# Kernel tuning notes

Hardware: AMD Instinct MI355X
Metric: run time of the kernel (lower is better)

## Reference

```python
import jax, jax.numpy as jnp
import numpy as np

N, C, P, M = 8, 20, 8732, 16
THRESHOLD, NEG_POS_RATIO, ALPHA = 0.5, 3, 1.0


def cxcy_to_xy(c):
    return jnp.concatenate([c[..., :2] - c[..., 2:] / 2.0, c[..., :2] + c[..., 2:] / 2.0], axis=-1)


def xy_to_cxcy(xy):
    return jnp.concatenate([(xy[..., :2] + xy[..., 2:]) / 2.0, xy[..., 2:] - xy[..., :2]], axis=-1)


def cxcy_to_gcxgcy(cxcy, priors):
    g_cxcy = (cxcy[..., :2] - priors[..., :2]) / (priors[..., 2:] / 10.0)
    g_wh = jnp.log(cxcy[..., 2:] / priors[..., 2:]) * 5.0
    return jnp.concatenate([g_cxcy, g_wh], axis=-1)


def jaccard(a, b):
    # a: (M,4), b: (P,4), boundary coords -> IoU (M,P)
    lo = jnp.maximum(a[:, None, :2], b[None, :, :2])
    hi = jnp.minimum(a[:, None, 2:], b[None, :, 2:])
    inter = jnp.prod(jnp.clip(hi - lo, 0.0), axis=-1)
    area_a = jnp.prod(a[:, 2:] - a[:, :2], axis=-1)
    area_b = jnp.prod(b[:, 2:] - b[:, :2], axis=-1)
    return inter / (area_a[:, None] + area_b[None, :] - inter)


def setup_inputs() -> dict:
    key = jax.random.key(0)
    k1, k2, k3, k4, k5, k6 = jax.random.split(key, 6)
    predicted_locs = jax.random.normal(k1, (N, C, P, 4), jnp.float32)
    predicted_scores = jax.random.normal(k2, (N, C, P, 2), jnp.float32)
    # valid ground-truth boundary boxes (x1<x2, y1<y2) in [0,1]
    ctr = jax.random.uniform(k3, (N, C, M, 2), minval=0.2, maxval=0.8)
    wh = jax.random.uniform(k4, (N, C, M, 2), minval=0.05, maxval=0.3)
    boxes = jnp.concatenate([ctr - wh / 2.0, ctr + wh / 2.0], axis=-1)
    # valid priors in cxcywh (w,h > 0 so log-encoding is finite)
    pctr = jax.random.uniform(k5, (P, 2), minval=0.05, maxval=0.95)
    pwh = jax.random.uniform(k6, (P, 2), minval=0.05, maxval=0.5)
    priors_cxcy = jnp.concatenate([pctr, pwh], axis=-1)
    labels = jnp.ones((N, C, M), jnp.int32)  # binary per-class head: object label = 1
    return {
        "predicted_locs": predicted_locs,
        "predicted_scores": predicted_scores,
        "boxes": boxes,
        "labels": labels,
        "priors_cxcy": priors_cxcy,
    }


def _forward(predicted_locs, predicted_scores, boxes, priors_cxcy, labels):
    n_classes = predicted_scores.shape[1]
    n_priors = predicted_scores.shape[2]
    priors_xy = cxcy_to_xy(priors_cxcy)

    def match(b, lab):
        # b: (M,4) boundary, lab: (M,) int
        ov = jaccard(b, priors_xy)                       # (M,P)
        obj_for_prior = jnp.argmax(ov, axis=0)           # (P,)
        ov_for_prior = jnp.max(ov, axis=0)               # (P,)
        prior_for_obj = jnp.argmax(ov, axis=1)           # (M,)
        # force each object to own its best prior
        obj_for_prior = obj_for_prior.at[prior_for_obj].set(jnp.arange(b.shape[0]))
        ov_for_prior = ov_for_prior.at[prior_for_obj].set(1.0)
        cls = jnp.where(ov_for_prior < THRESHOLD, 0, lab[obj_for_prior])  # (P,)
        tl = cxcy_to_gcxgcy(xy_to_cxcy(b[obj_for_prior]), priors_cxcy)    # (P,4)
        return tl, cls

    true_locs, true_classes = jax.vmap(jax.vmap(match))(boxes, labels)  # (N,C,P,4), (N,C,P)

    pos = true_classes != 0                      # (N,C,P)
    posf = pos.astype(predicted_locs.dtype)
    n_pos_bc = posf.sum(axis=2)                  # (N,C) positives per image per class
    n_pos_c = n_pos_bc.sum(axis=0)               # (C,)

    # localization: mean L1 over positive priors (4 coords each), per class
    l1 = jnp.abs(predicted_locs - true_locs).sum(-1) * posf   # (N,C,P)
    loc_loss_c = l1.sum(axis=(0, 2)) / jnp.maximum(n_pos_c * 4.0, 1.0)

    # per-prior binary cross entropy
    logp = jax.nn.log_softmax(predicted_scores, axis=-1)      # (N,C,P,2)
    ce = -jnp.take_along_axis(logp, true_classes[..., None], axis=-1)[..., 0]  # (N,C,P)
    conf_pos_c = (ce * posf).sum(axis=(0, 2))

    # hard negative mining: sort negatives desc per (image,class) row, keep top 3*n_pos
    ce_neg = jnp.where(pos, 0.0, ce)
    ce_neg_sorted = -jnp.sort(-ce_neg, axis=-1)               # (N,C,P) descending
    n_hard = NEG_POS_RATIO * n_pos_bc                         # (N,C)
    ranks = jnp.arange(n_priors, dtype=n_hard.dtype)
    hard_mask = ranks[None, None, :] < n_hard[..., None]
    conf_hard_c = (ce_neg_sorted * hard_mask).sum(axis=(0, 2))

    safe = jnp.maximum(n_pos_c, 1.0)
    loss_c = jnp.where(
        n_pos_c > 0,
        (conf_pos_c + conf_hard_c + ALPHA * loc_loss_c) / safe,
        0.0,
    ) / n_classes
    return loss_c.sum()


def reference(predicted_locs, predicted_scores, boxes, labels, priors_cxcy):
    return _forward(predicted_locs, predicted_scores, boxes, priors_cxcy, labels)
```

## Files before the change

### kernel.cpp

```cpp
#include <hip/hip_runtime.h>
#include <math.h>

#define NN 8
#define CC 20
#define PP 8732
#define MM 16
#define NPR 3
#define SPLIT 12
#define CH 728
#define ROWS (NN * CC)

__device__ __forceinline__ float fast_rcp(float x) { return __builtin_amdgcn_rcpf(x); }
__device__ __forceinline__ float rfl(float x) {
    return __uint_as_float(__builtin_amdgcn_readfirstlane(__float_as_uint(x)));
}

__device__ __forceinline__ float lse2(float a, float b) {
    float mx = fmaxf(a, b);
    float d  = fabsf(a - b);
    return mx + __logf(1.0f + __expf(-d));
}

#define ABLK 256
__global__ __launch_bounds__(ABLK) void mbox_p1(
    const float* __restrict__ locs, const float* __restrict__ scores,
    const float* __restrict__ boxes, const int* __restrict__ labels,
    const float* __restrict__ priors,
    unsigned char* __restrict__ pk8,
    unsigned long long* __restrict__ partials, float* __restrict__ cstats)
{
    const int row = blockIdx.x / SPLIT;
    const int chunk = blockIdx.x - row * SPLIT;
    const int tid = threadIdx.x, lane = tid & 63, wav = tid >> 6;

    __shared__ float s_bcx[MM], s_bcy[MM], s_bw[MM], s_bh[MM];
    __shared__ unsigned int s_pk[4 * MM];
    __shared__ float s_rf[4 * 3];

    float bx1[MM], by1[MM], bx2[MM], by2[MM], bar[MM];
    unsigned int labm = 0;
    {
        const float* bb = boxes + (size_t)row * MM * 4;
        const int*   lb = labels + (size_t)row * MM;
#pragma unroll
        for (int m = 0; m < MM; m++) {
            float x1 = rfl(bb[m * 4 + 0]), y1 = rfl(bb[m * 4 + 1]);
            float x2 = rfl(bb[m * 4 + 2]), y2 = rfl(bb[m * 4 + 3]);
            bx1[m] = x1; by1[m] = y1; bx2[m] = x2; by2[m] = y2;
            bar[m] = rfl((x2 - x1) * (y2 - y1));
            labm |= (lb[m] != 0 ? 1u : 0u) << m;
        }
        labm = __builtin_amdgcn_readfirstlane(labm);
    }
    if (tid < MM) {
        s_bcx[tid] = (bx1[tid] + bx2[tid]) * 0.5f;
        s_bcy[tid] = (by1[tid] + by2[tid]) * 0.5f;
        s_bw[tid]  = bx2[tid] - bx1[tid];
        s_bh[tid]  = by2[tid] - by1[tid];
    }
    __syncthreads();

    const float4* pri4 = (const float4*)priors;
    const float4* loc4 = (const float4*)(locs + (size_t)row * PP * 4);
    const float2* sc2  = (const float2*)(scores + (size_t)row * PP * 2);
    unsigned char* pk  = pk8 + (size_t)row * PP;

    unsigned int bestk[MM];
#pragma unroll
    for (int m = 0; m < MM; m++) bestk[m] = 0u;
    float l_np = 0.0f, l_l1 = 0.0f, l_cp = 0.0f;
    const int p0 = chunk * CH, p1e = min(p0 + CH, PP);

    float4 pr_next;
    if (p0 + tid < p1e) pr_next = pri4[p0 + tid];
    int it = 0;
    for (int p = p0 + tid; p < p1e; p += ABLK, ++it) {
        float4 pr = pr_next;
        if (p + ABLK < p1e) pr_next = pri4[p + ABLK];
        const unsigned int lowb = ((unsigned int)(7 - it) << 8) | (unsigned int)(255 - tid);
        float hw = pr.z * 0.5f, hh = pr.w * 0.5f;
        float px1 = pr.x - hw, py1 = pr.y - hh;
        float px2 = pr.x + hw, py2 = pr.y + hh;
        float area_b = (px2 - px1) * (py2 - py1);
        unsigned int bovk = 0u;
#pragma unroll
        for (int m = 0; m < MM; m++) {
            float dx = fminf(bx2[m], px2) - fmaxf(bx1[m], px1);
            float dy = fminf(by2[m], py2) - fmaxf(by1[m], py1);
            dx = fmaxf(dx, 0.0f); dy = fmaxf(dy, 0.0f);
            float inter = dx * dy;
            float den = (bar[m] + area_b) - inter;
            float iou = inter * fast_rcp(den);
            unsigned int ib = __float_as_uint(iou);
            unsigned int km = (ib & 0xFFFFFFF0u) | (unsigned int)(15 - m);
            bovk = max(bovk, km);
            unsigned int kp = (ib & 0xFFFFF800u) | lowb;
            bestk[m] = max(bestk[m], kp);
        }
        int bm = 15 - (int)(bovk & 15u);
        bool pos = (bovk >= 0x3F000000u) && (((labm >> bm) & 1u) != 0u);
        pk[p] = (unsigned char)((pos ? 16u : 0u) | (unsigned)bm);
        if (pos) {
            float2 sc = sc2[p];
            float4 pl = loc4[p];
            l_np += 1.0f;
            l_cp += lse2(sc.x, sc.y) - sc.y;
            float tx = (s_bcx[bm] - pr.x) * 10.0f / pr.z;
            float ty = (s_bcy[bm] - pr.y) * 10.0f / pr.w;
            float tw = __logf(s_bw[bm] / pr.z) * 5.0f;
            float th = __logf(s_bh[bm] / pr.w) * 5.0f;
            l_l1 += fabsf(pl.x - tx) + fabsf(pl.y - ty) + fabsf(pl.z - tw) + fabsf(pl.w - th);
        }
    }

#pragma unroll
    for (int m = 0; m < MM; m++) {
        unsigned int key = bestk[m];
#pragma unroll
        for (int off = 32; off; off >>= 1) {
            unsigned int o = __shfl_down(key, off);
            if (o > key) key = o;
        }
        if (lane == 0) s_pk[wav * MM + m] = key;
    }
#pragma unroll
    for (int off = 32; off; off >>= 1) {
        l_np += __shfl_down(l_np, off);
        l_l1 += __shfl_down(l_l1, off);
        l_cp += __shfl_down(l_cp, off);
    }
    if (lane == 0) { s_rf[wav * 3] = l_np; s_rf[wav * 3 + 1] = l_l1; s_rf[wav * 3 + 2] = l_cp; }
    __syncthreads();
    if (tid < MM) {
        unsigned int key = s_pk[tid];
        for (int w = 1; w < 4; w++) {
            unsigned int o = s_pk[w * MM + tid];
            if (o > key) key = o;
        }
        int tw  = 255 - (int)(key & 255u);
        int itw = 7 - (int)((key >> 8) & 7u);
        int pm  = p0 + itw * ABLK + tw;
        partials[((size_t)row * MM + tid) * SPLIT + chunk] =
            ((unsigned long long)(key & 0xFFFFF800u) << 32) |
            (unsigned int)(0x7fffffff - pm);
    }
    if (tid == 0) {
        float np = 0, l1 = 0, cp = 0;
        for (int w = 0; w < 4; w++) { np += s_rf[w * 3]; l1 += s_rf[w * 3 + 1]; cp += s_rf[w * 3 + 2]; }
        float* cs = cstats + ((size_t)row * SPLIT + chunk) * 3;
        cs[0] = np; cs[1] = l1; cs[2] = cp;
    }
}

#define CBLK 1024
#define EPT 9
__global__ __launch_bounds__(CBLK) void mbox_sel(
    const float* __restrict__ locs, const float* __restrict__ scores,
    const float* __restrict__ boxes, const int* __restrict__ labels,
    const float* __restrict__ priors,
    const unsigned char* __restrict__ pk8,
    const unsigned long long* __restrict__ partials,
    const float* __restrict__ cstats, float* __restrict__ rstats)
{
    const int row = blockIdx.x, tid = threadIdx.x, lane = tid & 63, wav = tid >> 6;
    __shared__ float s_bcx[MM], s_bcy[MM], s_bw[MM], s_bh[MM];
    __shared__ int s_lab[MM], s_pfo[MM], s_fp[MM];
    __shared__ float s_fv[MM], s_sum[3];
    __shared__ unsigned int s_hist[256];
    __shared__ unsigned int s_prefix, s_Kr, s_K;
    __shared__ float s_redf[16];
    __shared__ int s_redi[16];

    if (tid < MM) {
        s_fp[tid] = -1;
        const float* b = boxes + ((size_t)row * MM + tid) * 4;
        float x1 = b[0], y1 = b[1], x2 = b[2], y2 = b[3];
        s_bcx[tid] = (x1 + x2) * 0.5f; s_bcy[tid] = (y1 + y2) * 0.5f;
        s_bw[tid] = x2 - x1; s_bh[tid] = y2 - y1;
        s_lab[tid] = labels[row * MM + tid];
        const unsigned long long* pr = partials + ((size_t)row * MM + tid) * SPLIT;
        unsigned long long key = pr[0];
        for (int c = 1; c < SPLIT; c++) { unsigned long long o = pr[c]; if (o > key) key = o; }
        s_pfo[tid] = 0x7fffffff - (int)(unsigned)(key & 0xffffffffull);
    }
    if (tid >= 16 && tid < 19) {
        int j = tid - 16; float s = 0;
        for (int c = 0; c < SPLIT; c++) s += cstats[((size_t)row * SPLIT + c) * 3 + j];
        s_sum[j] = s;
    }
    __syncthreads();

    float d_np = 0, d_l1 = 0, d_cp = 0;
    if (tid < MM) {
        int p = s_pfo[tid];
        bool is_last = true;
        for (int mm = tid + 1; mm < MM; mm++) if (s_pfo[mm] == p) is_last = false;
        if (is_last) {
            const float4 pr = ((const float4*)priors)[p];
            const float4 pl = ((const float4*)(locs + (size_t)row * PP * 4))[p];
            const float2 sc = ((const float2*)(scores + (size_t)row * PP * 2))[p];
            float lse = lse2(sc.x, sc.y);
            unsigned int u = pk8[(size_t)row * PP + p];
            if (u & 16u) {
                int mo = u & 15;
                d_np -= 1.0f; d_cp -= (lse - sc.y);
                float tx = (s_bcx[mo] - pr.x) * 10.0f / pr.z;
                float ty = (s_bcy[mo] - pr.y) * 10.0f / pr.w;
                float tw = __logf(s_bw[mo] / pr.z) * 5.0f;
                float th = __logf(s_bh[mo] / pr.w) * 5.0f;
                d_l1 -= fabsf(pl.x - tx) + fabsf(pl.y - ty) + fabsf(pl.z - tw) + fabsf(pl.w - th);
            }
            if (s_lab[tid] != 0) {
                d_np += 1.0f; d_cp += (lse - sc.y);
                float tx = (s_bcx[tid] - pr.x) * 10.0f / pr.z;
                float ty = (s_bcy[tid] - pr.y) * 10.0f / pr.w;
                float tw = __logf(s_bw[tid] / pr.z) * 5.0f;
                float th = __logf(s_bh[tid] / pr.w) * 5.0f;
                d_l1 += fabsf(pl.x - tx) + fabsf(pl.y - ty) + fabsf(pl.z - tw) + fabsf(pl.w - th);
                s_fv[tid] = 0.0f;
            } else {
                s_fv[tid] = fmaxf(lse - sc.x, 0.0f);
            }
            s_fp[tid] = p;
        }
    }
    if (tid < 64) {
#pragma unroll
        for (int off = 32; off; off >>= 1) {
            d_np += __shfl_down(d_np, off);
            d_l1 += __shfl_down(d_l1, off);
            d_cp += __shfl_down(d_cp, off);
        }
        if (tid == 0) {
            float np = s_sum[0] + d_np;
            rstats[(size_t)row * 8 + 0] = np;
            rstats[(size_t)row * 8 + 1] = s_sum[1] + d_l1;
            rstats[(size_t)row * 8 + 2] = s_sum[2] + d_cp;
            int K = NPR * (int)(np + 0.5f);
            s_K = (K > 0) ? (unsigned)K : 0u;
            s_prefix = 0u;
            s_Kr = (K > 0) ? (unsigned)K : 0u;
        }
    }
    __syncthreads();

    const float2* sc2 = (const float2*)(scores + (size_t)row * PP * 2);
    const unsigned char* pk = pk8 + (size_t)row * PP;
    unsigned int uv[EPT];
#pragma unroll
    for (int k = 0; k < EPT; k++) {
        int p = tid + k * CBLK;
        if (p < PP) {
            unsigned int u8 = pk[p];
            float2 sc = sc2[p];
            float ce = (u8 & 16u) ? 0.0f : fmaxf(lse2(sc.x, sc.y) - sc.x, 0.0f);
            uv[k] = __float_as_uint(ce);
        } else uv[k] = 0u;
    }
    for (int t = 0; t < MM; t++) {
        int fp = s_fp[t];
        if (fp >= 0) {
            unsigned int fb = __float_as_uint(s_fv[t]);
#pragma unroll
            for (int k = 0; k < EPT; k++) if (tid + k * CBLK == fp) uv[k] = fb;
        }
    }

    const unsigned int K = s_K;
    unsigned int T = 0u;
    if (K > 0u && K < PP) {
        for (int pass = 0; pass < 4; pass++) {
            const int shift = 24 - 8 * pass;
            if (tid < 256) s_hist[tid] = 0u;
            __syncthreads();
            const unsigned int pref   = s_prefix;
            const unsigned int maskhi = (pass == 0) ? 0u : (0xffffffffu << (shift + 8));
#pragma unroll
            for (int k = 0; k < EPT; k++) {
                unsigned int u = uv[k];
                if ((u & maskhi) == pref) atomicAdd(&s_hist[(u >> shift) & 255u], 1u);
            }
            __syncthreads();
            if (wav == 0) {
                unsigned int Kr = s_Kr;
                unsigned int h0 = s_hist[lane * 4 + 0];
                unsigned int h1 = s_hist[lane * 4 + 1];
                unsigned int h2 = s_hist[lane * 4 + 2];
                unsigned int h3 = s_hist[lane * 4 + 3];
                unsigned int c3 = h3;
                unsigned int c2 = h3 + h2;
                unsigned int c1 = c2 + h1;
                unsigned int c0 = c1 + h0;
                unsigned int suf = c0;
#pragma unroll
                for (int off = 1; off < 64; off <<= 1) {
                    unsigned int o = __shfl_down(suf, off);
                    if (lane + off < 64) suf += o;
                }
                unsigned int above = suf - c0;
                int cand = -1;
                unsigned int G = 0;
                if      (c3 + above >= Kr) { cand = lane * 4 + 3; G = above + c3 - h3; }
                else if (c2 + above >= Kr) { cand = lane * 4 + 2; G = above + c2 - h2; }
                else if (c1 + above >= Kr) { cand = lane * 4 + 1; G = above + c1 - h1; }
                else if (c0 + above >= Kr) { cand = lane * 4 + 0; G = above + c0 - h0; }
                int best = cand;
#pragma unroll
                for (int off = 32; off; off >>= 1) best = max(best, __shfl_down(best, off));
                best = __shfl(best, 0);
                if (cand == best && cand >= 0) {
                    s_Kr = Kr - G;
                    s_prefix = pref | ((unsigned int)best << shift);
                }
            }
            __syncthreads();
        }
        T = s_prefix;
    }

    float sgt = 0.0f; int cgt = 0;
    if (K > 0u) {
#pragma unroll
        for (int k = 0; k < EPT; k++) {
            unsigned int u = uv[k];
            if (u > T) { sgt += __uint_as_float(u); cgt++; }
        }
    }
#pragma unroll
    for (int off = 32; off; off >>= 1) {
        sgt += __shfl_down(sgt, off);
        cgt += __shfl_down(cgt, off);
    }
    if (lane == 0) { s_redf[wav] = sgt; s_redi[wav] = cgt; }
    __syncthreads();
    if (tid == 0) {
        float s = 0; int cnt = 0;
        for (int w = 0; w < 16; w++) { s += s_redf[w]; cnt += s_redi[w]; }
        float chard = (K > 0u) ? (s + (float)(int)(K - (unsigned)cgt * 0u - (unsigned)cnt) * __uint_as_float(T)) : 0.0f;
        rstats[(size_t)row * 8 + 4] = chard;
    }
}

__global__ void mbox_finalize(const float* __restrict__ rstats, float* __restrict__ out) {
    int c = threadIdx.x;
    float loss = 0.0f;
    if (c < CC) {
        float np = 0, l1 = 0, cp = 0, ch = 0;
        for (int n = 0; n < NN; n++) {
            const float* s = rstats + ((size_t)(n * CC + c)) * 8;
            np += s[0]; l1 += s[1]; cp += s[2]; ch += s[4];
        }
        float loc = l1 / fmaxf(np * 4.0f, 1.0f);
        float val = (np > 0.0f) ? (cp + ch + loc) / fmaxf(np, 1.0f) : 0.0f;
        loss = val / (float)CC;
    }
#pragma unroll
    for (int off = 32; off; off >>= 1) loss += __shfl_down(loss, off);
    if (threadIdx.x == 0) out[0] = loss;
}

extern "C" void kernel_launch(void* const* d_in, const int* in_sizes, int n_in,
                              void* d_out, int out_size, void* d_ws, size_t ws_size,
                              hipStream_t stream) {
    const float* locs   = (const float*)d_in[0];
    const float* scores = (const float*)d_in[1];
    const float* boxes  = (const float*)d_in[2];
    const int*   labels = (const int*)d_in[3];
    const float* priors = (const float*)d_in[4];
    float* out = (float*)d_out;

    char* ws = (char*)d_ws;
    unsigned char* pk8           = (unsigned char*)ws;
    unsigned long long* partials = (unsigned long long*)(ws + 1397120);
    float* cstats                = (float*)(ws + 1642880);
    float* rstats                = (float*)(ws + 1665920);

    mbox_p1<<<ROWS * SPLIT, ABLK, 0, stream>>>(locs, scores, boxes, labels, priors,
                                               pk8, partials, cstats);
    mbox_sel<<<ROWS, CBLK, 0, stream>>>(locs, scores, boxes, labels, priors,
                                        pk8, partials, cstats, rstats);
    mbox_finalize<<<1, 64, 0, stream>>>(rstats, out);
}
```

Baseline: 126.4 us.

## Fuse selection and finalize into main kernel via last-block atomic counters

Merges the per-row selection kernel and the finalize kernel into the first kernel. The last of the SPLIT blocks for each row, detected with an atomic counter, does the row's hard-negative radix select, and the last row to finish computes the final loss. A small zeroing kernel resets the counters. This removes a kernel launch and the gap between kernels, but the selection now runs in a 256-thread block with 35 elements per thread instead of a 1024-thread block, so that serial tail step gets less parallelism and higher register pressure.

```diff
diff --git a/kernel.cpp b/kernel.cpp
--- a/kernel.cpp
+++ b/kernel.cpp
@@ -9,25 +9,31 @@
 #define SPLIT 12
 #define CH 728
 #define ROWS (NN * CC)
+#define ABLK 256
+#define EPT 35
 
 __device__ __forceinline__ float fast_rcp(float x) { return __builtin_amdgcn_rcpf(x); }
 __device__ __forceinline__ float rfl(float x) {
     return __uint_as_float(__builtin_amdgcn_readfirstlane(__float_as_uint(x)));
 }
-
 __device__ __forceinline__ float lse2(float a, float b) {
     float mx = fmaxf(a, b);
     float d  = fabsf(a - b);
     return mx + __logf(1.0f + __expf(-d));
 }
 
-#define ABLK 256
-__global__ __launch_bounds__(ABLK) void mbox_p1(
+__global__ void mbox_zero(unsigned int* __restrict__ c) {
+    if (threadIdx.x <= ROWS) c[threadIdx.x] = 0u;
+}
+
+__global__ __launch_bounds__(ABLK) void mbox_fused(
     const float* __restrict__ locs, const float* __restrict__ scores,
     const float* __restrict__ boxes, const int* __restrict__ labels,
     const float* __restrict__ priors,
     unsigned char* __restrict__ pk8,
-    unsigned long long* __restrict__ partials, float* __restrict__ cstats)
+    unsigned long long* __restrict__ partials, float* __restrict__ cstats,
+    float* __restrict__ rstats, unsigned int* __restrict__ counters,
+    float* __restrict__ out)
 {
     const int row = blockIdx.x / SPLIT;
     const int chunk = blockIdx.x - row * SPLIT;
@@ -36,6 +42,13 @@
     __shared__ float s_bcx[MM], s_bcy[MM], s_bw[MM], s_bh[MM];
     __shared__ unsigned int s_pk[4 * MM];
     __shared__ float s_rf[4 * 3];
+    __shared__ unsigned int s_last, s_fin;
+    __shared__ int s_pfo[MM], s_fp[MM];
+    __shared__ float s_fv[MM], s_sum[3];
+    __shared__ unsigned int s_hist[256];
+    __shared__ unsigned int s_prefix, s_Kr, s_K;
+    __shared__ float s_redf[4];
+    __shared__ int s_redi[4];
 
     float bx1[MM], by1[MM], bx2[MM], by2[MM], bar[MM];
     unsigned int labm = 0;
@@ -150,37 +163,23 @@
         float* cs = cstats + ((size_t)row * SPLIT + chunk) * 3;
         cs[0] = np; cs[1] = l1; cs[2] = cp;
     }
-}
-
-#define CBLK 1024
-#define EPT 9
-__global__ __launch_bounds__(CBLK) void mbox_sel(
-    const float* __restrict__ locs, const float* __restrict__ scores,
-    const float* __restrict__ boxes, const int* __restrict__ labels,
-    const float* __restrict__ priors,
-    const unsigned char* __restrict__ pk8,
-    const unsigned long long* __restrict__ partials,
-    const float* __restrict__ cstats, float* __restrict__ rstats)
-{
-    const int row = blockIdx.x, tid = threadIdx.x, lane = tid & 63, wav = tid >> 6;
-    __shared__ float s_bcx[MM], s_bcy[MM], s_bw[MM], s_bh[MM];
-    __shared__ int s_lab[MM], s_pfo[MM], s_fp[MM];
-    __shared__ float s_fv[MM], s_sum[3];
-    __shared__ unsigned int s_hist[256];
-    __shared__ unsigned int s_prefix, s_Kr, s_K;
-    __shared__ float s_redf[16];
-    __shared__ int s_redi[16];
+
+    __threadfence();
+    __syncthreads();
+    if (tid == 0) {
+        unsigned int old = __hip_atomic_fetch_add(&counters[row], 1u,
+                                                  __ATOMIC_ACQ_REL, __HIP_MEMORY_SCOPE_AGENT);
+        s_last = (old == SPLIT - 1) ? 1u : 0u;
+        if (s_last) __threadfence();
+    }
+    __syncthreads();
+    if (!s_last) return;
 
     if (tid < MM) {
         s_fp[tid] = -1;
-        const float* b = boxes + ((size_t)row * MM + tid) * 4;
-        float x1 = b[0], y1 = b[1], x2 = b[2], y2 = b[3];
-        s_bcx[tid] = (x1 + x2) * 0.5f; s_bcy[tid] = (y1 + y2) * 0.5f;
-        s_bw[tid] = x2 - x1; s_bh[tid] = y2 - y1;
-        s_lab[tid] = labels[row * MM + tid];
-        const unsigned long long* pr = partials + ((size_t)row * MM + tid) * SPLIT;
-        unsigned long long key = pr[0];
-        for (int c = 1; c < SPLIT; c++) { unsigned long long o = pr[c]; if (o > key) key = o; }
+        const unsigned long long* prt = partials + ((size_t)row * MM + tid) * SPLIT;
+        unsigned long long key = prt[0];
+        for (int c = 1; c < SPLIT; c++) { unsigned long long o = prt[c]; if (o > key) key = o; }
         s_pfo[tid] = 0x7fffffff - (int)(unsigned)(key & 0xffffffffull);
     }
     if (tid >= 16 && tid < 19) {
@@ -196,11 +195,11 @@
         bool is_last = true;
         for (int mm = tid + 1; mm < MM; mm++) if (s_pfo[mm] == p) is_last = false;
         if (is_last) {
-            const float4 pr = ((const float4*)priors)[p];
-            const float4 pl = ((const float4*)(locs + (size_t)row * PP * 4))[p];
-            const float2 sc = ((const float2*)(scores + (size_t)row * PP * 2))[p];
+            const float4 pr = pri4[p];
+            const float4 pl = loc4[p];
+            const float2 sc = sc2[p];
             float lse = lse2(sc.x, sc.y);
-            unsigned int u = pk8[(size_t)row * PP + p];
+            unsigned int u = pk[p];
             if (u & 16u) {
                 int mo = u & 15;
                 d_np -= 1.0f; d_cp -= (lse - sc.y);
@@ -210,7 +209,7 @@
                 float th = __logf(s_bh[mo] / pr.w) * 5.0f;
                 d_l1 -= fabsf(pl.x - tx) + fabsf(pl.y - ty) + fabsf(pl.z - tw) + fabsf(pl.w - th);
             }
-            if (s_lab[tid] != 0) {
+            if ((labm >> tid) & 1u) {
                 d_np += 1.0f; d_cp += (lse - sc.y);
                 float tx = (s_bcx[tid] - pr.x) * 10.0f / pr.z;
                 float ty = (s_bcy[tid] - pr.y) * 10.0f / pr.w;
@@ -244,12 +243,10 @@
     }
     __syncthreads();
 
-    const float2* sc2 = (const float2*)(scores + (size_t)row * PP * 2);
-    const unsigned char* pk = pk8 + (size_t)row * PP;
     unsigned int uv[EPT];
 #pragma unroll
     for (int k = 0; k < EPT; k++) {
-        int p = tid + k * CBLK;
+        int p = tid + k * ABLK;
         if (p < PP) {
             unsigned int u8 = pk[p];
             float2 sc = sc2[p];
@@ -262,7 +259,7 @@
         if (fp >= 0) {
             unsigned int fb = __float_as_uint(s_fv[t]);
 #pragma unroll
-            for (int k = 0; k < EPT; k++) if (tid + k * CBLK == fp) uv[k] = fb;
+            for (int k = 0; k < EPT; k++) if (tid + k * ABLK == fp) uv[k] = fb;
         }
     }
 
@@ -271,7 +268,7 @@
     if (K > 0u && K < PP) {
         for (int pass = 0; pass < 4; pass++) {
             const int shift = 24 - 8 * pass;
-            if (tid < 256) s_hist[tid] = 0u;
+            s_hist[tid] = 0u;
             __syncthreads();
             const unsigned int pref   = s_prefix;
             const unsigned int maskhi = (pass == 0) ? 0u : (0xffffffffu << (shift + 8));
@@ -335,28 +332,35 @@
     __syncthreads();
     if (tid == 0) {
         float s = 0; int cnt = 0;
-        for (int w = 0; w < 16; w++) { s += s_redf[w]; cnt += s_redi[w]; }
-        float chard = (K > 0u) ? (s + (float)(int)(K - (unsigned)cgt * 0u - (unsigned)cnt) * __uint_as_float(T)) : 0.0f;
+        for (int w = 0; w < 4; w++) { s += s_redf[w]; cnt += s_redi[w]; }
+        float chard = (K > 0u) ? (s + (float)(int)(K - (unsigned)cnt) * __uint_as_float(T)) : 0.0f;
         rstats[(size_t)row * 8 + 4] = chard;
-    }
-}
-
-__global__ void mbox_finalize(const float* __restrict__ rstats, float* __restrict__ out) {
-    int c = threadIdx.x;
-    float loss = 0.0f;
-    if (c < CC) {
-        float np = 0, l1 = 0, cp = 0, ch = 0;
-        for (int n = 0; n < NN; n++) {
-            const float* s = rstats + ((size_t)(n * CC + c)) * 8;
-            np += s[0]; l1 += s[1]; cp += s[2]; ch += s[4];
-        }
-        float loc = l1 / fmaxf(np * 4.0f, 1.0f);
-        float val = (np > 0.0f) ? (cp + ch + loc) / fmaxf(np, 1.0f) : 0.0f;
-        loss = val / (float)CC;
-    }
-#pragma unroll
-    for (int off = 32; off; off >>= 1) loss += __shfl_down(loss, off);
-    if (threadIdx.x == 0) out[0] = loss;
+        __threadfence();
+        unsigned int old2 = __hip_atomic_fetch_add(&counters[ROWS], 1u,
+                                                   __ATOMIC_ACQ_REL, __HIP_MEMORY_SCOPE_AGENT);
+        s_fin = (old2 == ROWS - 1) ? 1u : 0u;
+        if (s_fin) __threadfence();
+    }
+    __syncthreads();
+    if (!s_fin) return;
+
+    if (tid < 64) {
+        int c = tid;
+        float loss = 0.0f;
+        if (c < CC) {
+            float np = 0, l1 = 0, cp = 0, ch = 0;
+            for (int n = 0; n < NN; n++) {
+                const float* s = rstats + ((size_t)(n * CC + c)) * 8;
+                np += s[0]; l1 += s[1]; cp += s[2]; ch += s[4];
+            }
+            float loc = l1 / fmaxf(np * 4.0f, 1.0f);
+            float val = (np > 0.0f) ? (cp + ch + loc) / fmaxf(np, 1.0f) : 0.0f;
+            loss = val / (float)CC;
+        }
+#pragma unroll
+        for (int off = 32; off; off >>= 1) loss += __shfl_down(loss, off);
+        if (tid == 0) out[0] = loss;
+    }
 }
 
 extern "C" void kernel_launch(void* const* d_in, const int* in_sizes, int n_in,
@@ -374,10 +378,10 @@
     unsigned long long* partials = (unsigned long long*)(ws + 1397120);
     float* cstats                = (float*)(ws + 1642880);
     float* rstats                = (float*)(ws + 1665920);
-
-    mbox_p1<<<ROWS * SPLIT, ABLK, 0, stream>>>(locs, scores, boxes, labels, priors,
-                                               pk8, partials, cstats);
-    mbox_sel<<<ROWS, CBLK, 0, stream>>>(locs, scores, boxes, labels, priors,
-                                        pk8, partials, cstats, rstats);
-    mbox_finalize<<<1, 64, 0, stream>>>(rstats, out);
-}
+    unsigned int* counters       = (unsigned int*)(ws + 1671040);
+
+    mbox_zero<<<1, 256, 0, stream>>>(counters);
+    mbox_fused<<<ROWS * SPLIT, ABLK, 0, stream>>>(locs, scores, boxes, labels, priors,
+                                                  pk8, partials, cstats, rstats,
+                                                  counters, out);
+}
```

After: 367.5 us. +190.8%, slower.
